# Kernel tuning notes

Hardware: AMD Instinct MI355X
Metric: run time of the kernel (lower is better)

Reference implementation:

```python
import jax, jax.numpy as jnp
import numpy as np

B, L, H = 2, 1024, 1024   # batch, seq_len, hidden_size
NH, D, K = 16, 64, 4      # num_heads, head_dim, conv kernel
HD = NH * D


def setup_inputs() -> dict:
    key = jax.random.key(0)
    ks = jax.random.split(key, 12)
    s = 0.02  # LeCun-ish init scale as in the torch module
    return {
        "hidden_states": jax.random.normal(ks[0], (B, L, H), jnp.float32),
        "Wq": jax.random.normal(ks[1], (HD, H), jnp.float32) * s,
        "bq": jnp.zeros((HD,), jnp.float32),
        "Wk": jax.random.normal(ks[2], (HD, H), jnp.float32) * s,
        "bk": jnp.zeros((HD,), jnp.float32),
        "Wv": jax.random.normal(ks[3], (HD, H), jnp.float32) * s,
        "bv": jnp.zeros((HD,), jnp.float32),
        "Wa": jax.random.normal(ks[4], (NH, H), jnp.float32) * s,
        "Wb": jax.random.normal(ks[5], (NH, H), jnp.float32) * s,
        "Wconv": jax.random.normal(ks[6], (HD, 1, K), jnp.float32) * s,
        "Wo": jax.random.normal(ks[7], (H, HD), jnp.float32) * s,
        "bo": jnp.zeros((H,), jnp.float32),
    }


def _gated_delta(q, k, v, alpha, beta):
    # q,k,v: [B,L,NH,D]; alpha,beta: [B,L,NH]
    # S_t = S_{t-1} @ (alpha_t * (I - beta_t k_t k_t^T)) + beta_t v_t k_t^T ; o_t = S_t q_t
    eye = jnp.eye(q.shape[-1], dtype=q.dtype)

    def step(S, xs):
        q_t, k_t, v_t, a_t, b_t = xs  # [B,NH,D], [B,NH]
        kk = jnp.einsum('bhd,bhe->bhde', k_t, k_t)
        decay = a_t[..., None, None] * (eye - b_t[..., None, None] * kk)
        S = jnp.einsum('bhde,bhef->bhdf', S, decay) \
            + b_t[..., None, None] * jnp.einsum('bhd,bhe->bhde', v_t, k_t)
        o_t = jnp.einsum('bhde,bhe->bhd', S, q_t)
        return S, o_t

    xs = (jnp.moveaxis(q, 1, 0), jnp.moveaxis(k, 1, 0), jnp.moveaxis(v, 1, 0),
          jnp.moveaxis(alpha, 1, 0), jnp.moveaxis(beta, 1, 0))
    S0 = jnp.zeros((q.shape[0], q.shape[2], q.shape[3], q.shape[3]), q.dtype)
    _, outs = jax.lax.scan(step, S0, xs)  # [L,B,NH,D]
    return jnp.transpose(outs, (1, 2, 0, 3))  # [B,NH,L,D] (matches torch stack+transposes)


def reference(hidden_states, Wq, bq, Wk, bk, Wv, bv, Wa, Wb, Wconv, Wo, bo):
    Bc, Lc, Hc = hidden_states.shape
    q = (hidden_states @ Wq.T + bq).reshape(Bc, Lc, NH, D)
    k = (hidden_states @ Wk.T + bk).reshape(Bc, Lc, NH, D)
    v = (hidden_states @ Wv.T + bv).reshape(Bc, Lc, NH, D)
    alpha = jax.nn.sigmoid(hidden_states @ Wa.T)   # [B,L,NH]
    beta = jax.nn.softplus(hidden_states @ Wb.T)   # [B,L,NH]

    out = _gated_delta(q, k, v, alpha, beta)       # [B,NH,L,D]
    out = out.reshape(Bc, Lc, NH * D)              # replicates torch's reshape of [B,NH,L,D]
    x = jnp.transpose(out, (0, 2, 1))              # [B,HD,L]
    conv = jax.lax.conv_general_dilated(
        x, Wconv, window_strides=(1,), padding=[(K - 1, 0)],
        feature_group_count=NH * D, dimension_numbers=('NCH', 'OIH', 'NCH'))
    x = x + conv                                   # residual depthwise causal conv
    x = jnp.transpose(x, (0, 2, 1))                # [B,L,HD]
    return x @ Wo.T + bo                           # [B,L,H]; dropout is identity at eval
```

## Files before the change

### kernel.cpp

```cpp
#include <hip/hip_runtime.h>
#include <math.h>

#define BB 2
#define LL 1024
#define HH 1024
#define NH 16
#define DD 64
#define HD (NH * DD)
#define MM (BB * LL)
#define RCT 32
#define KEXT 3072
#define NBK 1152

typedef _Float16 f16x8 __attribute__((ext_vector_type(8)));
typedef _Float16 f16x4 __attribute__((ext_vector_type(4)));
typedef float f32x4 __attribute__((ext_vector_type(4)));

__device__ __forceinline__ void load_lds16(const void* g, void* l) {
    __builtin_amdgcn_global_load_lds(
        (const __attribute__((address_space(1))) void*)g,
        (__attribute__((address_space(3))) void*)l, 16, 0, 0);
}

__global__ __launch_bounds__(256) void convert_front(
    const float* __restrict__ hs,
    const float* __restrict__ Wq, const float* __restrict__ Wk,
    const float* __restrict__ Wv, const float* __restrict__ Wa,
    const float* __restrict__ Wb, const float* __restrict__ Wo,
    _Float16* __restrict__ Ae3, _Float16* __restrict__ Ah,
    _Float16* __restrict__ Bk, _Float16* __restrict__ Bqv,
    _Float16* __restrict__ Be2)
{
    const int blk = blockIdx.x;
    const int t = threadIdx.x;

    if (blk < 2048) {
        float4 x = *(const float4*)(hs + (size_t)blk * 1024 + t * 4);
        x.x *= 16.f; x.y *= 16.f; x.z *= 16.f; x.w *= 16.f;
        f16x4 h, l;
        h[0] = (_Float16)x.x; l[0] = (_Float16)(x.x - (float)h[0]);
        h[1] = (_Float16)x.y; l[1] = (_Float16)(x.y - (float)h[1]);
        h[2] = (_Float16)x.z; l[2] = (_Float16)(x.z - (float)h[2]);
        h[3] = (_Float16)x.w; l[3] = (_Float16)(x.w - (float)h[3]);
        _Float16* base = Ae3 + (size_t)blk * KEXT + t * 4;
        *(f16x4*)(base)        = h;
        *(f16x4*)(base + 1024) = l;
        *(f16x4*)(base + 2048) = h;
        *(f16x4*)(Ah + (size_t)blk * 1024 + t * 4) = h;
        return;
    }
    if (blk < 3200) {
        const int n = blk - 2048;
        const float* src = nullptr;
        if (n < 1024)      src = Wk + (size_t)n * 1024;
        else if (n < 1040) src = Wa + (size_t)(n - 1024) * 1024;
        else if (n < 1056) src = Wb + (size_t)(n - 1040) * 1024;
        float4 x = src ? *(const float4*)(src + t * 4)
                       : make_float4(0.f, 0.f, 0.f, 0.f);
        x.x *= 64.f; x.y *= 64.f; x.z *= 64.f; x.w *= 64.f;
        f16x4 h, l;
        h[0] = (_Float16)x.x; l[0] = (_Float16)(x.x - (float)h[0]);
        h[1] = (_Float16)x.y; l[1] = (_Float16)(x.y - (float)h[1]);
        h[2] = (_Float16)x.z; l[2] = (_Float16)(x.z - (float)h[2]);
        h[3] = (_Float16)x.w; l[3] = (_Float16)(x.w - (float)h[3]);
        _Float16* base = Bk + (size_t)n * KEXT + t * 4;
        *(f16x4*)(base)        = h;
        *(f16x4*)(base + 1024) = h;
        *(f16x4*)(base + 2048) = l;
        return;
    }
    if (blk < 5248) {
        const int n = blk - 3200;
        const float* src = (n < 1024) ? Wq + (size_t)n * 1024
                                      : Wv + (size_t)(n - 1024) * 1024;
        float4 x = *(const float4*)(src + t * 4);
        f16x4 h;
        h[0] = (_Float16)(x.x * 64.f);
        h[1] = (_Float16)(x.y * 64.f);
        h[2] = (_Float16)(x.z * 64.f);
        h[3] = (_Float16)(x.w * 64.f);
        *(f16x4*)(Bqv + (size_t)n * 1024 + t * 4) = h;
        return;
    }
    {
        const int n = blk - 5248;
        float4 x = *(const float4*)(Wo + (size_t)n * 1024 + t * 4);
        f16x4 h;
        h[0] = (_Float16)(x.x * 64.f);
        h[1] = (_Float16)(x.y * 64.f);
        h[2] = (_Float16)(x.z * 64.f);
        h[3] = (_Float16)(x.w * 64.f);
        *(f16x4*)(Be2 + (size_t)n * 1024 + t * 4) = h;
    }
}

__global__ __launch_bounds__(256) void mfma_gemm_k(
    const _Float16* __restrict__ Ae3, const _Float16* __restrict__ Bk,
    float* __restrict__ qkv, float* __restrict__ ab,
    const float* __restrict__ bk)
{
    __shared__ __align__(16) _Float16 As[2][128 * 32];
    __shared__ __align__(16) _Float16 Bs[2][64 * 32];

    const int tid = threadIdx.x;
    const int wave = tid >> 6;
    const int lane = tid & 63;
    const int bm = blockIdx.y * 128;
    const int bn = blockIdx.x * 64;
    const int wr = (wave >> 1) * 64;
    const int wc = (wave & 1) * 32;

    const int srow = lane >> 2;
    const int scol = (lane & 3) * 8;
    const _Float16* gA0 = Ae3 + (size_t)(bm + wave * 32 + srow) * KEXT + scol;
    const _Float16* gA1 = gA0 + (size_t)16 * KEXT;
    const _Float16* gB0 = Bk + (size_t)(bn + wave * 16 + srow) * KEXT + scol;
    _Float16* lA0_0 = &As[0][(wave * 32) * 32];
    _Float16* lA1_0 = &As[0][(wave * 32 + 16) * 32];
    _Float16* lB0_0 = &Bs[0][(wave * 16) * 32];
    _Float16* lA0_1 = &As[1][(wave * 32) * 32];
    _Float16* lA1_1 = &As[1][(wave * 32 + 16) * 32];
    _Float16* lB0_1 = &Bs[1][(wave * 16) * 32];

    const int fm = lane & 15;
    const int fq = (lane >> 4) * 8;

    f32x4 acc[4][2] = {};

    for (int k0 = 0; k0 < KEXT; k0 += 64) {
        load_lds16(gA0 + k0,      lA0_0);
        load_lds16(gA1 + k0,      lA1_0);
        load_lds16(gB0 + k0,      lB0_0);
        load_lds16(gA0 + k0 + 32, lA0_1);
        load_lds16(gA1 + k0 + 32, lA1_1);
        load_lds16(gB0 + k0 + 32, lB0_1);
        __syncthreads();

        #pragma unroll
        for (int s = 0; s < 2; ++s) {
            f16x8 a[4], b[2];
            #pragma unroll
            for (int mt = 0; mt < 4; ++mt)
                a[mt] = *(const f16x8*)&As[s][(wr + mt * 16 + fm) * 32 + fq];
            #pragma unroll
            for (int nt = 0; nt < 2; ++nt)
                b[nt] = *(const f16x8*)&Bs[s][(wc + nt * 16 + fm) * 32 + fq];
            #pragma unroll
            for (int mt = 0; mt < 4; ++mt)
                #pragma unroll
                for (int nt = 0; nt < 2; ++nt)
                    acc[mt][nt] = __builtin_amdgcn_mfma_f32_16x16x32_f16(
                        a[mt], b[nt], acc[mt][nt], 0, 0, 0);
        }
        __syncthreads();
    }

    const int rquad = (lane >> 4) * 4;
    #pragma unroll
    for (int mt = 0; mt < 4; ++mt) {
        #pragma unroll
        for (int nt = 0; nt < 2; ++nt) {
            const int col = bn + wc + nt * 16 + fm;
            #pragma unroll
            for (int i = 0; i < 4; ++i) {
                const int row = bm + wr + mt * 16 + rquad + i;
                float val = acc[mt][nt][i] * (1.0f / 1024.0f);
                if (col < 1024)
                    qkv[(size_t)row * 3072 + 1024 + col] = val + bk[col];
                else if (col < 1040)
                    ab[(size_t)row * 32 + (col - 1024)] =
                        1.f / (1.f + expf(-val));
                else if (col < 1056)
                    ab[(size_t)row * 32 + 16 + (col - 1040)] =
                        fmaxf(val, 0.f) + log1pf(expf(-fabsf(val)));
            }
        }
    }
}

__global__ __launch_bounds__(256) void mfma_gemm_qv(
    const _Float16* __restrict__ Ah, const _Float16* __restrict__ Bqv,
    float* __restrict__ qkv,
    const float* __restrict__ bq, const float* __restrict__ bv)
{
    __shared__ __align__(16) _Float16 As[2][128 * 32];
    __shared__ __align__(16) _Float16 Bs[2][128 * 32];

    const int tid = threadIdx.x;
    const int wave = tid >> 6;
    const int lane = tid & 63;
    const int bm = blockIdx.y * 128;
    const int bn = blockIdx.x * 128;
    const int wr = (wave >> 1) * 64;
    const int wc = (wave & 1) * 64;

    const int srow = lane >> 2;
    const int scol = (lane & 3) * 8;
    const _Float16* gA0 = Ah + (size_t)(bm + wave * 32 + srow) * 1024 + scol;
    const _Float16* gA1 = gA0 + (size_t)16 * 1024;
    const _Float16* gB0 = Bqv + (size_t)(bn + wave * 32 + srow) * 1024 + scol;
    const _Float16* gB1 = gB0 + (size_t)16 * 1024;
    _Float16* lA0_0 = &As[0][(wave * 32) * 32];
    _Float16* lA1_0 = &As[0][(wave * 32 + 16) * 32];
    _Float16* lB0_0 = &Bs[0][(wave * 32) * 32];
    _Float16* lB1_0 = &Bs[0][(wave * 32 + 16) * 32];
    _Float16* lA0_1 = &As[1][(wave * 32) * 32];
    _Float16* lA1_1 = &As[1][(wave * 32 + 16) * 32];
    _Float16* lB0_1 = &Bs[1][(wave * 32) * 32];
    _Float16* lB1_1 = &Bs[1][(wave * 32 + 16) * 32];

    const int fm = lane & 15;
    const int fq = (lane >> 4) * 8;

    f32x4 acc[4][4] = {};

    for (int k0 = 0; k0 < 1024; k0 += 64) {
        load_lds16(gA0 + k0,      lA0_0);
        load_lds16(gA1 + k0,      lA1_0);
        load_lds16(gB0 + k0,      lB0_0);
        load_lds16(gB1 + k0,      lB1_0);
        load_lds16(gA0 + k0 + 32, lA0_1);
        load_lds16(gA1 + k0 + 32, lA1_1);
        load_lds16(gB0 + k0 + 32, lB0_1);
        load_lds16(gB1 + k0 + 32, lB1_1);
        __syncthreads();

        #pragma unroll
        for (int s = 0; s < 2; ++s) {
            f16x8 a[4], b[4];
            #pragma unroll
            for (int mt = 0; mt < 4; ++mt)
                a[mt] = *(const f16x8*)&As[s][(wr + mt * 16 + fm) * 32 + fq];
            #pragma unroll
            for (int nt = 0; nt < 4; ++nt)
                b[nt] = *(const f16x8*)&Bs[s][(wc + nt * 16 + fm) * 32 + fq];
            #pragma unroll
            for (int mt = 0; mt < 4; ++mt)
                #pragma unroll
                for (int nt = 0; nt < 4; ++nt)
                    acc[mt][nt] = __builtin_amdgcn_mfma_f32_16x16x32_f16(
                        a[mt], b[nt], acc[mt][nt], 0, 0, 0);
        }
        __syncthreads();
    }

    const int rquad = (lane >> 4) * 4;
    #pragma unroll
    for (int mt = 0; mt < 4; ++mt) {
        #pragma unroll
        for (int nt = 0; nt < 4; ++nt) {
            const int col = bn + wc + nt * 16 + fm;
            #pragma unroll
            for (int i = 0; i < 4; ++i) {
                const int row = bm + wr + mt * 16 + rquad + i;
                float val = acc[mt][nt][i] * (1.0f / 1024.0f);
                if (col < 1024)
                    qkv[(size_t)row * 3072 + col] = val + bq[col];
                else
                    qkv[(size_t)row * 3072 + 1024 + col] = val + bv[col - 1024];
            }
        }
    }
}

__global__ __launch_bounds__(256) void mfma_gemm_out(
    const _Float16* __restrict__ Ae2, const _Float16* __restrict__ Be2,
    float* __restrict__ outp, const float* __restrict__ bo)
{
    __shared__ __align__(16) _Float16 As[2][128 * 32];
    __shared__ __align__(16) _Float16 Bs[2][64 * 32];

    const int tid = threadIdx.x;
    const int wave = tid >> 6;
    const int lane = tid & 63;
    const int bm = blockIdx.y * 128;
    const int bn = blockIdx.x * 64;
    const int wr = (wave >> 1) * 64;
    const int wc = (wave & 1) * 32;

    const int srow = lane >> 2;
    const int scol = (lane & 3) * 8;
    const _Float16* gA0 = Ae2 + (size_t)(bm + wave * 32 + srow) * 1024 + scol;
    const _Float16* gA1 = gA0 + (size_t)16 * 1024;
    const _Float16* gB0 = Be2 + (size_t)(bn + wave * 16 + srow) * 1024 + scol;
    _Float16* lA0_0 = &As[0][(wave * 32) * 32];
    _Float16* lA1_0 = &As[0][(wave * 32 + 16) * 32];
    _Float16* lB0_0 = &Bs[0][(wave * 16) * 32];
    _Float16* lA0_1 = &As[1][(wave * 32) * 32];
    _Float16* lA1_1 = &As[1][(wave * 32 + 16) * 32];
    _Float16* lB0_1 = &Bs[1][(wave * 16) * 32];

    const int fm = lane & 15;
    const int fq = (lane >> 4) * 8;

    f32x4 acc[4][2] = {};

    for (int k0 = 0; k0 < 1024; k0 += 64) {
        load_lds16(gA0 + k0,      lA0_0);
        load_lds16(gA1 + k0,      lA1_0);
        load_lds16(gB0 + k0,      lB0_0);
        load_lds16(gA0 + k0 + 32, lA0_1);
        load_lds16(gA1 + k0 + 32, lA1_1);
        load_lds16(gB0 + k0 + 32, lB0_1);
        __syncthreads();

        #pragma unroll
        for (int s = 0; s < 2; ++s) {
            f16x8 a[4], b[2];
            #pragma unroll
            for (int mt = 0; mt < 4; ++mt)
                a[mt] = *(const f16x8*)&As[s][(wr + mt * 16 + fm) * 32 + fq];
            #pragma unroll
            for (int nt = 0; nt < 2; ++nt)
                b[nt] = *(const f16x8*)&Bs[s][(wc + nt * 16 + fm) * 32 + fq];
            #pragma unroll
            for (int mt = 0; mt < 4; ++mt)
                #pragma unroll
                for (int nt = 0; nt < 2; ++nt)
                    acc[mt][nt] = __builtin_amdgcn_mfma_f32_16x16x32_f16(
                        a[mt], b[nt], acc[mt][nt], 0, 0, 0);
        }
        __syncthreads();
    }

    const int rquad = (lane >> 4) * 4;
    #pragma unroll
    for (int mt = 0; mt < 4; ++mt) {
        #pragma unroll
        for (int nt = 0; nt < 2; ++nt) {
            const int col = bn + wc + nt * 16 + fm;
            #pragma unroll
            for (int i = 0; i < 4; ++i) {
                const int row = bm + wr + mt * 16 + rquad + i;
                outp[(size_t)row * 1024 + col] = acc[mt][nt][i] * 64.f + bo[col];
            }
        }
    }
}

template <int CTRL>
__device__ __forceinline__ float dpp_addf(float x) {
    int y = __builtin_amdgcn_update_dpp(0, __builtin_bit_cast(int, x),
                                        CTRL, 0xF, 0xF, true);
    return x + __builtin_bit_cast(float, y);
}
__device__ __forceinline__ float red16(float x) {
    x = dpp_addf<0xB1>(x);
    x = dpp_addf<0x4E>(x);
    x = dpp_addf<0x124>(x);
    x = dpp_addf<0x128>(x);
    return x;
}

__global__ __launch_bounds__(64) void gdn_recurrence(
    const float* __restrict__ qkv, const float* __restrict__ ab,
    float* __restrict__ att)
{
    __shared__ __align__(16) float ks[2][RCT][64];
    __shared__ __align__(16) float qs[2][RCT][64];
    __shared__ __align__(16) float vs_[2][RCT][4];
    __shared__ __align__(16) float gab[2][RCT][2];

    const int blk = blockIdx.x;
    const int bh = blk & 31;
    const int s  = blk >> 5;
    const int b  = bh >> 4;
    const int h  = bh & 15;
    const int lane = threadIdx.x;
    const int rl = lane >> 4;
    const int el = lane & 15;
    const int e0 = el * 4;
    const int r0 = s * 4;

    const float* qb  = qkv + (size_t)b * LL * 3072 + h * 64;
    const float* kb  = qb + 1024;
    const float* vb  = qb + 2048 + r0;
    const float* abp = ab + (size_t)b * LL * 32 + h;
    float* op = att + ((size_t)(b * NH + h) * DD + r0 + rl) * LL;

    const int st = lane >> 4;
    const int sd = (lane & 15) * 4;

    float S0 = 0.f, S1 = 0.f, S2 = 0.f, S3 = 0.f;

    {
        const size_t ro = (size_t)st * 3072 + sd;
        #pragma unroll
        for (int m = 0; m < 8; ++m) {
            load_lds16(kb + ro + (size_t)m * 4 * 3072, &ks[0][m * 4][0]);
            load_lds16(qb + ro + (size_t)m * 4 * 3072, &qs[0][m * 4][0]);
        }
        float4 pv = make_float4(0.f,0.f,0.f,0.f);
        if (lane < RCT) pv = *(const float4*)(vb + (size_t)lane * 3072);
        float pab = (lane < 32) ? abp[(size_t)lane * 32]
                                : abp[(size_t)(lane - 32) * 32 + 16];
        if (lane < RCT) *(float4*)&vs_[0][lane][0] = pv;
        if (lane < 32) gab[0][lane][0] = pab;
        else           gab[0][lane - 32][1] = pab;
    }
    __syncthreads();

    const int NCHUNK = LL / RCT;
    for (int c = 0; c < NCHUNK; ++c) {
        const int cur = c & 1, nxt = cur ^ 1;
        const bool more = (c + 1 < NCHUNK);

        float4 pv = make_float4(0.f,0.f,0.f,0.f);
        float pab = 0.f;
        if (more) {
            const size_t t0 = (size_t)(c + 1) * RCT;
            const size_t ro = (t0 + st) * 3072 + sd;
            #pragma unroll
            for (int m = 0; m < 8; ++m) {
                load_lds16(kb + ro + (size_t)m * 4 * 3072, &ks[nxt][m * 4][0]);
                load_lds16(qb + ro + (size_t)m * 4 * 3072, &qs[nxt][m * 4][0]);
            }
            if (lane < RCT) pv = *(const float4*)(vb + (t0 + lane) * 3072);
            pab = (lane < 32) ? abp[(t0 + lane) * 32]
                              : abp[(t0 + lane - 32) * 32 + 16];
        }

        float4 kc = *(const float4*)&ks[cur][0][e0];
        float4 qc = *(const float4*)&qs[cur][0][e0];
        float vc = vs_[cur][0][rl];
        float2 abc = *(const float2*)&gab[cur][0][0];
        float ac = abc.x;
        float bc = abc.y;

        float o0 = 0.f, o1 = 0.f, o2 = 0.f;
        #pragma unroll 4
        for (int t = 0; t < RCT; ++t) {
            const int tn = (t + 1) & (RCT - 1);
            float4 kn = *(const float4*)&ks[cur][tn][e0];
            float4 qn = *(const float4*)&qs[cur][tn][e0];
            const float vn = vs_[cur][tn][rl];
            const float2 abn = *(const float2*)&gab[cur][tn][0];

            float p0 = fmaf(S1, kc.y, S0 * kc.x);
            float p1 = fmaf(S3, kc.w, S2 * kc.z);
            float sk = red16(p0 + p1);

            const float cf = bc * fmaf(-ac, sk, vc);

            S0 = fmaf(ac, S0, cf * kc.x);
            S1 = fmaf(ac, S1, cf * kc.y);
            S2 = fmaf(ac, S2, cf * kc.z);
            S3 = fmaf(ac, S3, cf * kc.w);

            float q0 = fmaf(S1, qc.y, S0 * qc.x);
            float q1 = fmaf(S3, qc.w, S2 * qc.z);
            float o = red16(q0 + q1);

            const int ph = t & 3;
            if (ph == 0) o0 = o;
            else if (ph == 1) o1 = o;
            else if (ph == 2) o2 = o;
            else if (el == 0)
                *(float4*)(op + c * RCT + t - 3) = make_float4(o0, o1, o2, o);

            kc = kn; qc = qn; vc = vn; ac = abn.x; bc = abn.y;
        }

        if (more) {
            if (lane < RCT) *(float4*)&vs_[nxt][lane][0] = pv;
            if (lane < 32) gab[nxt][lane][0] = pab;
            else           gab[nxt][lane - 32][1] = pab;
        }
        __syncthreads();
    }
}

__global__ __launch_bounds__(256) void conv_convert(
    const float* __restrict__ att, const float* __restrict__ Wconv,
    _Float16* __restrict__ Ae2)
{
    __shared__ float yt[112][68];
    const int lb = blockIdx.x;
    const int h  = blockIdx.y;
    const int b  = blockIdx.z;
    const int tid = threadIdx.x;

    {
        const int d = tid >> 2;
        const int part = tid & 3;
        const float* src  = att + ((size_t)(b * NH + h) * DD + d) * LL;
        const float* srcm = src - (size_t)DD * LL;
        #pragma unroll
        for (int m = 0; m < 7; ++m) {
            const int off = (part * 7 + m) * 4;
            const int lg = lb * 64 - 48 + off;
            float4 v;
            if (lg >= 0)      v = *(const float4*)(src + lg);
            else if (h > 0)   v = *(const float4*)(srcm + lg + 1024);
            else              v = make_float4(0.f, 0.f, 0.f, 0.f);
            yt[off + 0][d] = v.x; yt[off + 1][d] = v.y;
            yt[off + 2][d] = v.z; yt[off + 3][d] = v.w;
        }
    }
    __syncthreads();

    float4 w[4];
    #pragma unroll
    for (int k = 0; k < 4; ++k)
        w[k] = ((const float4*)Wconv)[tid * 4 + k];

    const int d0 = (tid & 15) * 4;
    const int lq = tid >> 4;
    const float sc = 1.f / 4096.f;

    #pragma unroll
    for (int rr = 0; rr < 4; ++rr) {
        const int ll = rr * 16 + lq;
        float y0[4], y1[4], y2[4], y3[4];
        *(float4*)y0 = *(const float4*)&yt[ll +  0][d0];
        *(float4*)y1 = *(const float4*)&yt[ll + 16][d0];
        *(float4*)y2 = *(const float4*)&yt[ll + 32][d0];
        *(float4*)y3 = *(const float4*)&yt[ll + 48][d0];
        f16x4 hi;
        #pragma unroll
        for (int k = 0; k < 4; ++k) {
            float acc = y3[k];
            acc = fmaf(w[k].x, y0[k], acc);
            acc = fmaf(w[k].y, y1[k], acc);
            acc = fmaf(w[k].z, y2[k], acc);
            acc = fmaf(w[k].w, y3[k], acc);
            hi[k] = (_Float16)(acc * sc);
        }
        const size_t row = (size_t)b * 1024 + h * 64 + lb * 4 + rr;
        *(f16x4*)(Ae2 + row * 1024 + tid * 4) = hi;
    }
}

extern "C" void kernel_launch(void* const* d_in, const int* in_sizes, int n_in,
                              void* d_out, int out_size, void* d_ws, size_t ws_size,
                              hipStream_t stream)
{
    const float* hs    = (const float*)d_in[0];
    const float* Wq    = (const float*)d_in[1];
    const float* bq    = (const float*)d_in[2];
    const float* Wk    = (const float*)d_in[3];
    const float* bk    = (const float*)d_in[4];
    const float* Wv    = (const float*)d_in[5];
    const float* bv    = (const float*)d_in[6];
    const float* Wa    = (const float*)d_in[7];
    const float* Wb    = (const float*)d_in[8];
    const float* Wconv = (const float*)d_in[9];
    const float* Wo    = (const float*)d_in[10];
    const float* bo    = (const float*)d_in[11];
    float* out = (float*)d_out;

    char* w = (char*)d_ws;
    float* qkv = (float*)w;        w += (size_t)MM * 3072 * 4;
    float* att = (float*)w;        w += (size_t)MM * 1024 * 4;
    float* ab  = (float*)w;        w += (size_t)MM * 32 * 4;
    _Float16* Ae3 = (_Float16*)w;  w += (size_t)MM * KEXT * 2;
    _Float16* Ah  = (_Float16*)w;  w += (size_t)MM * 1024 * 2;
    _Float16* Bk  = (_Float16*)w;  w += (size_t)NBK * KEXT * 2;
    _Float16* Bqv = (_Float16*)w;  w += (size_t)2048 * 1024 * 2;
    _Float16* Ae2 = (_Float16*)w;  w += (size_t)MM * 1024 * 2;
    _Float16* Be2 = (_Float16*)w;  w += (size_t)1024 * 1024 * 2;

    hipLaunchKernelGGL(convert_front, dim3(6272), dim3(256), 0, stream,
                       hs, Wq, Wk, Wv, Wa, Wb, Wo, Ae3, Ah, Bk, Bqv, Be2);

    hipLaunchKernelGGL(mfma_gemm_k, dim3(NBK / 64, MM / 128), dim3(256), 0, stream,
                       Ae3, Bk, qkv, ab, bk);

    hipLaunchKernelGGL(mfma_gemm_qv, dim3(2048 / 128, MM / 128), dim3(256), 0, stream,
                       Ah, Bqv, qkv, bq, bv);

    hipLaunchKernelGGL(gdn_recurrence, dim3(512), dim3(64), 0, stream, qkv, ab, att);

    hipLaunchKernelGGL(conv_convert, dim3(16, 16, BB), dim3(256), 0, stream,
                       att, Wconv, Ae2);

    hipLaunchKernelGGL(mfma_gemm_out, dim3(1024 / 64, MM / 128), dim3(256), 0, stream,
                       Ae2, Be2, out, bo);
}
```

Measured before the change: 310.6 us.

## Merge k and qv projection GEMMs into one launch; prefetch recurrence inputs two steps ahead

Combines the two projection GEMM kernels into a single launch of 544 blocks. The first 288 blocks handle the K/alpha/beta GEMM and the rest handle the Q/V GEMM, which removes a launch boundary and lets both GEMMs fill the GPU together. The recurrence loop now prefetches k, q, v and gates from LDS two steps ahead into a 4-slot register ring instead of one step ahead, to hide LDS latency on the serial chain. The costs are more LDS for the k blocks (Bs grows to 128 rows), which may lower occupancy, and extra registers in the recurrence.

```diff
diff --git a/kernel.cpp b/kernel.cpp
--- a/kernel.cpp
+++ b/kernel.cpp
@@ -94,170 +94,158 @@
     }
 }
 
-__global__ __launch_bounds__(256) void mfma_gemm_k(
+__global__ __launch_bounds__(256) void mfma_gemm_proj(
     const _Float16* __restrict__ Ae3, const _Float16* __restrict__ Bk,
+    const _Float16* __restrict__ Ah, const _Float16* __restrict__ Bqv,
     float* __restrict__ qkv, float* __restrict__ ab,
-    const float* __restrict__ bk)
+    const float* __restrict__ bq, const float* __restrict__ bk,
+    const float* __restrict__ bv)
 {
     __shared__ __align__(16) _Float16 As[2][128 * 32];
-    __shared__ __align__(16) _Float16 Bs[2][64 * 32];
-
+    __shared__ __align__(16) _Float16 Bs[2][128 * 32];
+
+    const int blk = blockIdx.x;
     const int tid = threadIdx.x;
     const int wave = tid >> 6;
     const int lane = tid & 63;
-    const int bm = blockIdx.y * 128;
-    const int bn = blockIdx.x * 64;
-    const int wr = (wave >> 1) * 64;
-    const int wc = (wave & 1) * 32;
-
     const int srow = lane >> 2;
     const int scol = (lane & 3) * 8;
-    const _Float16* gA0 = Ae3 + (size_t)(bm + wave * 32 + srow) * KEXT + scol;
-    const _Float16* gA1 = gA0 + (size_t)16 * KEXT;
-    const _Float16* gB0 = Bk + (size_t)(bn + wave * 16 + srow) * KEXT + scol;
-    _Float16* lA0_0 = &As[0][(wave * 32) * 32];
-    _Float16* lA1_0 = &As[0][(wave * 32 + 16) * 32];
-    _Float16* lB0_0 = &Bs[0][(wave * 16) * 32];
-    _Float16* lA0_1 = &As[1][(wave * 32) * 32];
-    _Float16* lA1_1 = &As[1][(wave * 32 + 16) * 32];
-    _Float16* lB0_1 = &Bs[1][(wave * 16) * 32];
-
     const int fm = lane & 15;
     const int fq = (lane >> 4) * 8;
-
-    f32x4 acc[4][2] = {};
-
-    for (int k0 = 0; k0 < KEXT; k0 += 64) {
-        load_lds16(gA0 + k0,      lA0_0);
-        load_lds16(gA1 + k0,      lA1_0);
-        load_lds16(gB0 + k0,      lB0_0);
-        load_lds16(gA0 + k0 + 32, lA0_1);
-        load_lds16(gA1 + k0 + 32, lA1_1);
-        load_lds16(gB0 + k0 + 32, lB0_1);
-        __syncthreads();
-
-        #pragma unroll
-        for (int s = 0; s < 2; ++s) {
-            f16x8 a[4], b[2];
-            #pragma unroll
-            for (int mt = 0; mt < 4; ++mt)
-                a[mt] = *(const f16x8*)&As[s][(wr + mt * 16 + fm) * 32 + fq];
-            #pragma unroll
-            for (int nt = 0; nt < 2; ++nt)
-                b[nt] = *(const f16x8*)&Bs[s][(wc + nt * 16 + fm) * 32 + fq];
-            #pragma unroll
-            for (int mt = 0; mt < 4; ++mt)
+    const int rquad = (lane >> 4) * 4;
+
+    if (blk < 288) {
+        const int bm = (blk / 18) * 128;
+        const int bn = (blk % 18) * 64;
+        const int wr = (wave >> 1) * 64;
+        const int wc = (wave & 1) * 32;
+
+        const _Float16* gA0 = Ae3 + (size_t)(bm + wave * 32 + srow) * KEXT + scol;
+        const _Float16* gA1 = gA0 + (size_t)16 * KEXT;
+        const _Float16* gB0 = Bk + (size_t)(bn + wave * 16 + srow) * KEXT + scol;
+        _Float16* lA0_0 = &As[0][(wave * 32) * 32];
+        _Float16* lA1_0 = &As[0][(wave * 32 + 16) * 32];
+        _Float16* lB0_0 = &Bs[0][(wave * 16) * 32];
+        _Float16* lA0_1 = &As[1][(wave * 32) * 32];
+        _Float16* lA1_1 = &As[1][(wave * 32 + 16) * 32];
+        _Float16* lB0_1 = &Bs[1][(wave * 16) * 32];
+
+        f32x4 acc[4][2] = {};
+
+        for (int k0 = 0; k0 < KEXT; k0 += 64) {
+            load_lds16(gA0 + k0,      lA0_0);
+            load_lds16(gA1 + k0,      lA1_0);
+            load_lds16(gB0 + k0,      lB0_0);
+            load_lds16(gA0 + k0 + 32, lA0_1);
+            load_lds16(gA1 + k0 + 32, lA1_1);
+            load_lds16(gB0 + k0 + 32, lB0_1);
+            __syncthreads();
+
+            #pragma unroll
+            for (int s = 0; s < 2; ++s) {
+                f16x8 a[4], b[2];
+                #pragma unroll
+                for (int mt = 0; mt < 4; ++mt)
+                    a[mt] = *(const f16x8*)&As[s][(wr + mt * 16 + fm) * 32 + fq];
                 #pragma unroll
                 for (int nt = 0; nt < 2; ++nt)
-                    acc[mt][nt] = __builtin_amdgcn_mfma_f32_16x16x32_f16(
-                        a[mt], b[nt], acc[mt][nt], 0, 0, 0);
-        }
-        __syncthreads();
-    }
-
-    const int rquad = (lane >> 4) * 4;
-    #pragma unroll
-    for (int mt = 0; mt < 4; ++mt) {
-        #pragma unroll
-        for (int nt = 0; nt < 2; ++nt) {
-            const int col = bn + wc + nt * 16 + fm;
-            #pragma unroll
-            for (int i = 0; i < 4; ++i) {
-                const int row = bm + wr + mt * 16 + rquad + i;
-                float val = acc[mt][nt][i] * (1.0f / 1024.0f);
-                if (col < 1024)
-                    qkv[(size_t)row * 3072 + 1024 + col] = val + bk[col];
-                else if (col < 1040)
-                    ab[(size_t)row * 32 + (col - 1024)] =
-                        1.f / (1.f + expf(-val));
-                else if (col < 1056)
-                    ab[(size_t)row * 32 + 16 + (col - 1040)] =
-                        fmaxf(val, 0.f) + log1pf(expf(-fabsf(val)));
+                    b[nt] = *(const f16x8*)&Bs[s][(wc + nt * 16 + fm) * 32 + fq];
+                #pragma unroll
+                for (int mt = 0; mt < 4; ++mt)
+                    #pragma unroll
+                    for (int nt = 0; nt < 2; ++nt)
+                        acc[mt][nt] = __builtin_amdgcn_mfma_f32_16x16x32_f16(
+                            a[mt], b[nt], acc[mt][nt], 0, 0, 0);
             }
-        }
-    }
-}
-
-__global__ __launch_bounds__(256) void mfma_gemm_qv(
-    const _Float16* __restrict__ Ah, const _Float16* __restrict__ Bqv,
-    float* __restrict__ qkv,
-    const float* __restrict__ bq, const float* __restrict__ bv)
-{
-    __shared__ __align__(16) _Float16 As[2][128 * 32];
-    __shared__ __align__(16) _Float16 Bs[2][128 * 32];
-
-    const int tid = threadIdx.x;
-    const int wave = tid >> 6;
-    const int lane = tid & 63;
-    const int bm = blockIdx.y * 128;
-    const int bn = blockIdx.x * 128;
-    const int wr = (wave >> 1) * 64;
-    const int wc = (wave & 1) * 64;
-
-    const int srow = lane >> 2;
-    const int scol = (lane & 3) * 8;
-    const _Float16* gA0 = Ah + (size_t)(bm + wave * 32 + srow) * 1024 + scol;
-    const _Float16* gA1 = gA0 + (size_t)16 * 1024;
-    const _Float16* gB0 = Bqv + (size_t)(bn + wave * 32 + srow) * 1024 + scol;
-    const _Float16* gB1 = gB0 + (size_t)16 * 1024;
-    _Float16* lA0_0 = &As[0][(wave * 32) * 32];
-    _Float16* lA1_0 = &As[0][(wave * 32 + 16) * 32];
-    _Float16* lB0_0 = &Bs[0][(wave * 32) * 32];
-    _Float16* lB1_0 = &Bs[0][(wave * 32 + 16) * 32];
-    _Float16* lA0_1 = &As[1][(wave * 32) * 32];
-    _Float16* lA1_1 = &As[1][(wave * 32 + 16) * 32];
-    _Float16* lB0_1 = &Bs[1][(wave * 32) * 32];
-    _Float16* lB1_1 = &Bs[1][(wave * 32 + 16) * 32];
-
-    const int fm = lane & 15;
-    const int fq = (lane >> 4) * 8;
-
-    f32x4 acc[4][4] = {};
-
-    for (int k0 = 0; k0 < 1024; k0 += 64) {
-        load_lds16(gA0 + k0,      lA0_0);
-        load_lds16(gA1 + k0,      lA1_0);
-        load_lds16(gB0 + k0,      lB0_0);
-        load_lds16(gB1 + k0,      lB1_0);
-        load_lds16(gA0 + k0 + 32, lA0_1);
-        load_lds16(gA1 + k0 + 32, lA1_1);
-        load_lds16(gB0 + k0 + 32, lB0_1);
-        load_lds16(gB1 + k0 + 32, lB1_1);
-        __syncthreads();
-
-        #pragma unroll
-        for (int s = 0; s < 2; ++s) {
-            f16x8 a[4], b[4];
-            #pragma unroll
-            for (int mt = 0; mt < 4; ++mt)
-                a[mt] = *(const f16x8*)&As[s][(wr + mt * 16 + fm) * 32 + fq];
-            #pragma unroll
-            for (int nt = 0; nt < 4; ++nt)
-                b[nt] = *(const f16x8*)&Bs[s][(wc + nt * 16 + fm) * 32 + fq];
-            #pragma unroll
-            for (int mt = 0; mt < 4; ++mt)
+            __syncthreads();
+        }
+
+        #pragma unroll
+        for (int mt = 0; mt < 4; ++mt) {
+            #pragma unroll
+            for (int nt = 0; nt < 2; ++nt) {
+                const int col = bn + wc + nt * 16 + fm;
+                #pragma unroll
+                for (int i = 0; i < 4; ++i) {
+                    const int row = bm + wr + mt * 16 + rquad + i;
+                    float val = acc[mt][nt][i] * (1.0f / 1024.0f);
+                    if (col < 1024)
+                        qkv[(size_t)row * 3072 + 1024 + col] = val + bk[col];
+                    else if (col < 1040)
+                        ab[(size_t)row * 32 + (col - 1024)] =
+                            1.f / (1.f + expf(-val));
+                    else if (col < 1056)
+                        ab[(size_t)row * 32 + 16 + (col - 1040)] =
+                            fmaxf(val, 0.f) + log1pf(expf(-fabsf(val)));
+                }
+            }
+        }
+    } else {
+        const int n = blk - 288;
+        const int bm = (n / 16) * 128;
+        const int bn = (n % 16) * 128;
+        const int wr = (wave >> 1) * 64;
+        const int wc = (wave & 1) * 64;
+
+        const _Float16* gA0 = Ah + (size_t)(bm + wave * 32 + srow) * 1024 + scol;
+        const _Float16* gA1 = gA0 + (size_t)16 * 1024;
+        const _Float16* gB0 = Bqv + (size_t)(bn + wave * 32 + srow) * 1024 + scol;
+        const _Float16* gB1 = gB0 + (size_t)16 * 1024;
+        _Float16* lA0_0 = &As[0][(wave * 32) * 32];
+        _Float16* lA1_0 = &As[0][(wave * 32 + 16) * 32];
+        _Float16* lB0_0 = &Bs[0][(wave * 32) * 32];
+        _Float16* lB1_0 = &Bs[0][(wave * 32 + 16) * 32];
+        _Float16* lA0_1 = &As[1][(wave * 32) * 32];
+        _Float16* lA1_1 = &As[1][(wave * 32 + 16) * 32];
+        _Float16* lB0_1 = &Bs[1][(wave * 32) * 32];
+        _Float16* lB1_1 = &Bs[1][(wave * 32 + 16) * 32];
+
+        f32x4 acc[4][4] = {};
+
+        for (int k0 = 0; k0 < 1024; k0 += 64) {
+            load_lds16(gA0 + k0,      lA0_0);
+            load_lds16(gA1 + k0,      lA1_0);
+            load_lds16(gB0 + k0,      lB0_0);
+            load_lds16(gB1 + k0,      lB1_0);
+            load_lds16(gA0 + k0 + 32, lA0_1);
+            load_lds16(gA1 + k0 + 32, lA1_1);
+            load_lds16(gB0 + k0 + 32, lB0_1);
+            load_lds16(gB1 + k0 + 32, lB1_1);
+            __syncthreads();
+
+            #pragma unroll
+            for (int s = 0; s < 2; ++s) {
+                f16x8 a[4], b[4];
+                #pragma unroll
+                for (int mt = 0; mt < 4; ++mt)
+                    a[mt] = *(const f16x8*)&As[s][(wr + mt * 16 + fm) * 32 + fq];
                 #pragma unroll
                 for (int nt = 0; nt < 4; ++nt)
-                    acc[mt][nt] = __builtin_amdgcn_mfma_f32_16x16x32_f16(
-                        a[mt], b[nt], acc[mt][nt], 0, 0, 0);
-        }
-        __syncthreads();
-    }
-
-    const int rquad = (lane >> 4) * 4;
-    #pragma unroll
-    for (int mt = 0; mt < 4; ++mt) {
-        #pragma unroll
-        for (int nt = 0; nt < 4; ++nt) {
-            const int col = bn + wc + nt * 16 + fm;
-            #pragma unroll
-            for (int i = 0; i < 4; ++i) {
-                const int row = bm + wr + mt * 16 + rquad + i;
-                float val = acc[mt][nt][i] * (1.0f / 1024.0f);
-                if (col < 1024)
-                    qkv[(size_t)row * 3072 + col] = val + bq[col];
-                else
-                    qkv[(size_t)row * 3072 + 1024 + col] = val + bv[col - 1024];
+                    b[nt] = *(const f16x8*)&Bs[s][(wc + nt * 16 + fm) * 32 + fq];
+                #pragma unroll
+                for (int mt = 0; mt < 4; ++mt)
+                    #pragma unroll
+                    for (int nt = 0; nt < 4; ++nt)
+                        acc[mt][nt] = __builtin_amdgcn_mfma_f32_16x16x32_f16(
+                            a[mt], b[nt], acc[mt][nt], 0, 0, 0);
+            }
+            __syncthreads();
+        }
+
+        #pragma unroll
+        for (int mt = 0; mt < 4; ++mt) {
+            #pragma unroll
+            for (int nt = 0; nt < 4; ++nt) {
+                const int col = bn + wc + nt * 16 + fm;
+                #pragma unroll
+                for (int i = 0; i < 4; ++i) {
+                    const int row = bm + wr + mt * 16 + rquad + i;
+                    float val = acc[mt][nt][i] * (1.0f / 1024.0f);
+                    if (col < 1024)
+                        qkv[(size_t)row * 3072 + col] = val + bq[col];
+                    else
+                        qkv[(size_t)row * 3072 + 1024 + col] = val + bv[col - 1024];
+                }
             }
         }
     }
@@ -420,21 +408,31 @@
                               : abp[(t0 + lane - 32) * 32 + 16];
         }
 
-        float4 kc = *(const float4*)&ks[cur][0][e0];
-        float4 qc = *(const float4*)&qs[cur][0][e0];
-        float vc = vs_[cur][0][rl];
-        float2 abc = *(const float2*)&gab[cur][0][0];
-        float ac = abc.x;
-        float bc = abc.y;
+        float4 kr[4], qr[4];
+        float vr[4];
+        float2 abr[4];
+        #pragma unroll
+        for (int i = 0; i < 2; ++i) {
+            kr[i] = *(const float4*)&ks[cur][i][e0];
+            qr[i] = *(const float4*)&qs[cur][i][e0];
+            vr[i] = vs_[cur][i][rl];
+            abr[i] = *(const float2*)&gab[cur][i][0];
+        }
 
         float o0 = 0.f, o1 = 0.f, o2 = 0.f;
         #pragma unroll 4
         for (int t = 0; t < RCT; ++t) {
-            const int tn = (t + 1) & (RCT - 1);
-            float4 kn = *(const float4*)&ks[cur][tn][e0];
-            float4 qn = *(const float4*)&qs[cur][tn][e0];
-            const float vn = vs_[cur][tn][rl];
-            const float2 abn = *(const float2*)&gab[cur][tn][0];
+            const int tf = (t + 2 < RCT) ? t + 2 : RCT - 1;
+            kr[(t + 2) & 3] = *(const float4*)&ks[cur][tf][e0];
+            qr[(t + 2) & 3] = *(const float4*)&qs[cur][tf][e0];
+            vr[(t + 2) & 3] = vs_[cur][tf][rl];
+            abr[(t + 2) & 3] = *(const float2*)&gab[cur][tf][0];
+
+            const float4 kc = kr[t & 3];
+            const float4 qc = qr[t & 3];
+            const float vc = vr[t & 3];
+            const float ac = abr[t & 3].x;
+            const float bc = abr[t & 3].y;
 
             float p0 = fmaf(S1, kc.y, S0 * kc.x);
             float p1 = fmaf(S3, kc.w, S2 * kc.z);
@@ -457,8 +455,6 @@
             else if (ph == 2) o2 = o;
             else if (el == 0)
                 *(float4*)(op + c * RCT + t - 3) = make_float4(o0, o1, o2, o);
-
-            kc = kn; qc = qn; vc = vn; ac = abn.x; bc = abn.y;
         }
 
         if (more) {
@@ -563,11 +559,8 @@
     hipLaunchKernelGGL(convert_front, dim3(6272), dim3(256), 0, stream,
                        hs, Wq, Wk, Wv, Wa, Wb, Wo, Ae3, Ah, Bk, Bqv, Be2);
 
-    hipLaunchKernelGGL(mfma_gemm_k, dim3(NBK / 64, MM / 128), dim3(256), 0, stream,
-                       Ae3, Bk, qkv, ab, bk);
-
-    hipLaunchKernelGGL(mfma_gemm_qv, dim3(2048 / 128, MM / 128), dim3(256), 0, stream,
-                       Ah, Bqv, qkv, bq, bv);
+    hipLaunchKernelGGL(mfma_gemm_proj, dim3(544), dim3(256), 0, stream,
+                       Ae3, Bk, Ah, Bqv, qkv, ab, bq, bk, bv);
 
     hipLaunchKernelGGL(gdn_recurrence, dim3(512), dim3(64), 0, stream, qkv, ab, att);
 
```

Result: faster. 294.2 us (-5.3%).
